# Kernel optimization log

Hardware: AMD Instinct MI355X
Metric: run time of the kernel (lower is better)

## Reference

```python
import jax, jax.numpy as jnp
import numpy as np
from jax import lax

B, T, P, H, O = 64, 96, 256, 128, 24  # batch, seq_len, num_points, hidden_dim, pred_len


def setup_inputs() -> dict:
    key = jax.random.key(0)
    ks = jax.random.split(key, 7)
    s = 1.0 / np.sqrt(H)  # torch LSTM/Linear default init scale
    return {
        "x": jax.random.normal(ks[0], (B, T, P, 1), dtype=jnp.float32),
        "W_ih": jax.random.uniform(ks[1], (P, 4 * H, 1), jnp.float32, -s, s),
        "W_hh": jax.random.uniform(ks[2], (P, 4 * H, H), jnp.float32, -s, s),
        "b_ih": jax.random.uniform(ks[3], (P, 4 * H), jnp.float32, -s, s),
        "b_hh": jax.random.uniform(ks[4], (P, 4 * H), jnp.float32, -s, s),
        "W_fc": jax.random.uniform(ks[5], (P, O, H), jnp.float32, -s, s),
        "b_fc": jax.random.uniform(ks[6], (P, O), jnp.float32, -s, s),
    }


def reference(x, W_ih, W_hh, b_ih, b_hh, W_fc, b_fc):
    # x: [B, T, P, F]; model uses only feature 0
    xs = x[..., 0]  # [B, T, P]
    # input_dim == 1, so input-to-gate contribution is a scaled broadcast of W_ih
    # precompute for all timesteps: [T, B, P, 4H]
    gx = jnp.einsum("btp,pg->tbpg", xs, W_ih[:, :, 0]) + (b_ih + b_hh)

    def step(carry, gxt):
        h, c = carry  # [B, P, H] each
        gates = gxt + jnp.einsum("bph,pgh->bpg", h, W_hh)  # [B, P, 4H]
        i, f, g, o = jnp.split(gates, 4, axis=-1)  # torch gate order i,f,g,o
        i = jax.nn.sigmoid(i)
        f = jax.nn.sigmoid(f)
        g = jnp.tanh(g)
        o = jax.nn.sigmoid(o)
        c = f * c + i * g
        h = o * jnp.tanh(c)
        return (h, c), None

    h0 = jnp.zeros((B, P, H), dtype=x.dtype)
    (h, _), _ = lax.scan(step, (h0, h0), gx)
    # per-point Linear on final hidden state: [B, P, O]
    out = jnp.einsum("bph,poh->bpo", h, W_fc) + b_fc
    # original stacks point outputs on last dim -> [B, pred_len, P]
    return jnp.transpose(out, (0, 2, 1))
```

## Files before the change

kernel.cpp:

```cpp
#include <hip/hip_runtime.h>
#include <hip/hip_bf16.h>

#define Bdim 64
#define Tdim 96
#define Pdim 256
#define Hdim 128
#define Gdim 512
#define Odim 24
#define BH   32
#define WROW 132

typedef _Float16 f16x8 __attribute__((ext_vector_type(8)));
typedef float    f32x16 __attribute__((ext_vector_type(16)));

union H8 { uint2 u2[2]; unsigned short s[8]; _Float16 h[8]; f16x8 v; };
union HS { _Float16 h; unsigned short s; };

__device__ __forceinline__ float exp2_fast(float x) {
#if __has_builtin(__builtin_amdgcn_exp2f)
    return __builtin_amdgcn_exp2f(x);
#else
    return __expf(x * 0.6931471805599453f);
#endif
}

__global__ __launch_bounds__(512, 4)
void lstm_fused(const float* __restrict__ x,
                const float* __restrict__ W_ih,
                const float* __restrict__ W_hh,
                const float* __restrict__ b_ih,
                const float* __restrict__ b_hh,
                const float* __restrict__ W_fc,
                const float* __restrict__ b_fc,
                float* __restrict__ out)
{
    __shared__ unsigned short hl[2][BH * WROW];

    const int p    = blockIdx.x >> 1;
    const int half = blockIdx.x & 1;
    const int tid  = threadIdx.x;
    const int w    = tid >> 6;
    const int l    = tid & 63;
    const int l31  = l & 31;
    const int hi   = l >> 5;

    const float L1 = 1.4426950408889634f;
    const float L2 = 2.0f * L1;

    for (int i = tid; i < 2 * BH * WROW; i += 512) ((unsigned short*)hl)[i] = 0;

    f16x8 afr[2][9];
    #pragma unroll
    for (int mt = 0; mt < 2; ++mt) {
        const int rp   = w * 64 + mt * 32 + l31;
        const int orow = ((rp & 3) << 7) | (rp >> 2);
        const float sc = ((rp & 3) == 2) ? L2 : L1;
        const float* rowp = W_hh + (size_t)p * Gdim * Hdim + (size_t)orow * Hdim;
        #pragma unroll
        for (int ks = 0; ks < 8; ++ks) {
            int k0 = ks * 16 + hi * 8;
            float4 va = *(const float4*)(rowp + k0);
            float4 vb = *(const float4*)(rowp + k0 + 4);
            H8 u;
            u.h[0] = (_Float16)(sc * va.x); u.h[1] = (_Float16)(sc * va.y);
            u.h[2] = (_Float16)(sc * va.z); u.h[3] = (_Float16)(sc * va.w);
            u.h[4] = (_Float16)(sc * vb.x); u.h[5] = (_Float16)(sc * vb.y);
            u.h[6] = (_Float16)(sc * vb.z); u.h[7] = (_Float16)(sc * vb.w);
            afr[mt][ks] = u.v;
        }
        H8 u9;
        #pragma unroll
        for (int j = 0; j < 8; ++j) u9.s[j] = 0;
        if (hi == 0) {
            u9.h[0] = (_Float16)(sc * W_ih[(size_t)p * Gdim + orow]);
            u9.h[1] = (_Float16)(sc * (b_ih[(size_t)p * Gdim + orow] +
                                       b_hh[(size_t)p * Gdim + orow]));
        }
        afr[mt][8] = u9.v;
    }

    float cre[2][4];
    #pragma unroll
    for (int mt = 0; mt < 2; ++mt)
        #pragma unroll
        for (int q = 0; q < 4; ++q) cre[mt][q] = 0.f;

    const float* xp = x + (size_t)((half * BH + l31) * Tdim) * Pdim + p;
    float xv = xp[0];

    __syncthreads();

    int cur = 0;
    for (int t = 0; t < Tdim; ++t) {
        float xn = (t + 1 < Tdim) ? xp[(size_t)(t + 1) * Pdim] : 0.f;

        f32x16 acc[2];
        #pragma unroll
        for (int j = 0; j < 16; ++j) { acc[0][j] = 0.f; acc[1][j] = 0.f; }

        const char* hbase = (const char*)hl[cur];
        #pragma unroll
        for (int ks = 0; ks < 8; ++ks) {
            int boff = l31 * (WROW * 2) + ks * 32 + hi * 16;
            H8 b0;
            b0.u2[0] = *(const uint2*)(hbase + boff);
            b0.u2[1] = *(const uint2*)(hbase + boff + 8);
            acc[0] = __builtin_amdgcn_mfma_f32_32x32x16_f16(afr[0][ks], b0.v, acc[0], 0, 0, 0);
            acc[1] = __builtin_amdgcn_mfma_f32_32x32x16_f16(afr[1][ks], b0.v, acc[1], 0, 0, 0);
        }
        {
            H8 b0;
            #pragma unroll
            for (int j = 0; j < 8; ++j) b0.s[j] = 0;
            if (hi == 0) { b0.h[0] = (_Float16)xv; b0.h[1] = (_Float16)1.0f; }
            acc[0] = __builtin_amdgcn_mfma_f32_32x32x16_f16(afr[0][8], b0.v, acc[0], 0, 0, 0);
            acc[1] = __builtin_amdgcn_mfma_f32_32x32x16_f16(afr[1][8], b0.v, acc[1], 0, 0, 0);
        }

        unsigned short* hw = hl[cur ^ 1];
        #pragma unroll
        for (int mt = 0; mt < 2; ++mt) {
            #pragma unroll
            for (int q = 0; q < 4; ++q) {
                float yi = acc[mt][4 * q + 0];
                float yf = acc[mt][4 * q + 1];
                float yg = acc[mt][4 * q + 2];
                float yo = acc[mt][4 * q + 3];
                float Ef = exp2_fast(-yf);
                float Ei = exp2_fast(-yi);
                float Eg = exp2_fast(yg);
                float t1 = 1.0f + Ef;
                float t2 = 1.0f + Ei;
                float t3 = Eg + 1.0f;
                float t4 = Eg - 1.0f;
                float den = (t1 * t2) * t3;
                float ct2 = cre[mt][q] * t2;
                float g4  = L2 * t4;
                float num = __builtin_fmaf(ct2, t3, g4 * t1);
                float cn  = num * __builtin_amdgcn_rcpf(den);
                cn = fminf(60.0f, fmaxf(-60.0f, cn));
                cre[mt][q] = cn;
                float Eo = exp2_fast(-yo);
                float Ec = exp2_fast(cn);
                float den2 = (1.0f + Eo) * (Ec + 1.0f);
                float hv = (Ec - 1.0f) * __builtin_amdgcn_rcpf(den2);
                HS hs; hs.h = (_Float16)hv;
                int k = w * 16 + mt * 8 + 2 * q + hi;
                hw[l31 * WROW + k] = hs.s;
            }
        }

        __syncthreads();
        cur ^= 1;
        xv = xn;
    }

    const float* wfc = W_fc + (size_t)p * Odim * Hdim;
    const float* bfc = b_fc + (size_t)p * Odim;
    const unsigned short* hf = hl[cur];
    for (int i = tid; i < BH * Odim; i += 512) {
        int o = i % Odim;
        int b = i / Odim;
        float s = bfc[o];
        const float* wr = wfc + o * Hdim;
        const unsigned short* hr = hf + b * WROW;
        #pragma unroll 8
        for (int k2 = 0; k2 < Hdim; ++k2) {
            HS hs; hs.s = hr[k2];
            s = __builtin_fmaf(wr[k2], (float)hs.h, s);
        }
        int bg = half * BH + b;
        out[(size_t)bg * Odim * Pdim + (size_t)o * Pdim + p] = s;
    }
}

extern "C" void kernel_launch(void* const* d_in, const int* in_sizes, int n_in,
                              void* d_out, int out_size, void* d_ws, size_t ws_size,
                              hipStream_t stream) {
    const float* x    = (const float*)d_in[0];
    const float* W_ih = (const float*)d_in[1];
    const float* W_hh = (const float*)d_in[2];
    const float* b_ih = (const float*)d_in[3];
    const float* b_hh = (const float*)d_in[4];
    const float* W_fc = (const float*)d_in[5];
    const float* b_fc = (const float*)d_in[6];
    float* out = (float*)d_out;

    lstm_fused<<<dim3(2 * Pdim), dim3(512), 0, stream>>>(x, W_ih, W_hh, b_ih, b_hh, W_fc, b_fc, out);
}
```

Before: 419.3 us.

## Merge batch halves into one block and interleave GEMM with the other half's epilogue

```diff
diff --git a/kernel.cpp b/kernel.cpp
--- a/kernel.cpp
+++ b/kernel.cpp
@@ -24,7 +24,7 @@
 #endif
 }
 
-__global__ __launch_bounds__(512, 4)
+__global__ __launch_bounds__(1024, 4)
 void lstm_fused(const float* __restrict__ x,
                 const float* __restrict__ W_ih,
                 const float* __restrict__ W_hh,
@@ -34,25 +34,22 @@
                 const float* __restrict__ b_fc,
                 float* __restrict__ out)
 {
-    __shared__ unsigned short hl[2][BH * WROW];
+    __shared__ unsigned short hs[2][2][BH * WROW];
 
-    const int p    = blockIdx.x >> 1;
-    const int half = blockIdx.x & 1;
-    const int tid  = threadIdx.x;
-    const int w    = tid >> 6;
-    const int l    = tid & 63;
-    const int l31  = l & 31;
-    const int hi   = l >> 5;
+    const int p   = blockIdx.x;
+    const int tid = threadIdx.x;
+    const int w   = tid >> 6;
+    const int l31 = tid & 31;
+    const int hi  = (tid >> 5) & 1;
 
     const float L1 = 1.4426950408889634f;
     const float L2 = 2.0f * L1;
 
-    for (int i = tid; i < 2 * BH * WROW; i += 512) ((unsigned short*)hl)[i] = 0;
+    for (int i = tid; i < 2 * 2 * BH * WROW; i += 1024) ((unsigned short*)hs)[i] = 0;
 
-    f16x8 afr[2][9];
-    #pragma unroll
-    for (int mt = 0; mt < 2; ++mt) {
-        const int rp   = w * 64 + mt * 32 + l31;
+    f16x8 afr[9];
+    {
+        const int rp   = w * 32 + l31;
         const int orow = ((rp & 3) << 7) | (rp >> 2);
         const float sc = ((rp & 3) == 2) ? L2 : L1;
         const float* rowp = W_hh + (size_t)p * Gdim * Hdim + (size_t)orow * Hdim;
@@ -66,7 +63,7 @@
             u.h[2] = (_Float16)(sc * va.z); u.h[3] = (_Float16)(sc * va.w);
             u.h[4] = (_Float16)(sc * vb.x); u.h[5] = (_Float16)(sc * vb.y);
             u.h[6] = (_Float16)(sc * vb.z); u.h[7] = (_Float16)(sc * vb.w);
-            afr[mt][ks] = u.v;
+            afr[ks] = u.v;
         }
         H8 u9;
         #pragma unroll
@@ -76,101 +73,101 @@
             u9.h[1] = (_Float16)(sc * (b_ih[(size_t)p * Gdim + orow] +
                                        b_hh[(size_t)p * Gdim + orow]));
         }
-        afr[mt][8] = u9.v;
+        afr[8] = u9.v;
     }
 
-    float cre[2][4];
-    #pragma unroll
-    for (int mt = 0; mt < 2; ++mt)
+    auto do_gemm = [&](const unsigned short* hb, float xv) -> f32x16 {
+        f32x16 a;
         #pragma unroll
-        for (int q = 0; q < 4; ++q) cre[mt][q] = 0.f;
+        for (int j = 0; j < 16; ++j) a[j] = 0.f;
+        const char* hbase = (const char*)hb;
+        #pragma unroll
+        for (int ks = 0; ks < 8; ++ks) {
+            int boff = l31 * (WROW * 2) + ks * 32 + hi * 16;
+            H8 bb;
+            bb.u2[0] = *(const uint2*)(hbase + boff);
+            bb.u2[1] = *(const uint2*)(hbase + boff + 8);
+            a = __builtin_amdgcn_mfma_f32_32x32x16_f16(afr[ks], bb.v, a, 0, 0, 0);
+        }
+        H8 bg;
+        #pragma unroll
+        for (int j = 0; j < 8; ++j) bg.s[j] = 0;
+        if (hi == 0) { bg.h[0] = (_Float16)xv; bg.h[1] = (_Float16)1.0f; }
+        a = __builtin_amdgcn_mfma_f32_32x32x16_f16(afr[8], bg.v, a, 0, 0, 0);
+        return a;
+    };
 
-    const float* xp = x + (size_t)((half * BH + l31) * Tdim) * Pdim + p;
-    float xv = xp[0];
+    auto do_ep = [&](const f32x16& a, float* cr, unsigned short* hw) {
+        #pragma unroll
+        for (int q = 0; q < 4; ++q) {
+            float yi = a[4 * q + 0];
+            float yf = a[4 * q + 1];
+            float yg = a[4 * q + 2];
+            float yo = a[4 * q + 3];
+            float Ef = exp2_fast(-yf);
+            float Ei = exp2_fast(-yi);
+            float Eg = exp2_fast(yg);
+            float t1 = 1.0f + Ef;
+            float t2 = 1.0f + Ei;
+            float t3 = Eg + 1.0f;
+            float t4 = Eg - 1.0f;
+            float den = (t1 * t2) * t3;
+            float num = __builtin_fmaf(cr[q] * t2, t3, (L2 * t4) * t1);
+            float cn  = num * __builtin_amdgcn_rcpf(den);
+            cn = fminf(60.0f, fmaxf(-60.0f, cn));
+            cr[q] = cn;
+            float Eo = exp2_fast(-yo);
+            float Ec = exp2_fast(cn);
+            float hv = (Ec - 1.0f) * __builtin_amdgcn_rcpf((1.0f + Eo) * (Ec + 1.0f));
+            HS s2; s2.h = (_Float16)hv;
+            hw[l31 * WROW + (w * 8 + 2 * q + hi)] = s2.s;
+        }
+    };
+
+    float cre0[4] = {0.f, 0.f, 0.f, 0.f};
+    float cre1[4] = {0.f, 0.f, 0.f, 0.f};
+
+    const float* xp0 = x + (size_t)((0 * BH + l31) * Tdim) * Pdim + p;
+    const float* xp1 = x + (size_t)((1 * BH + l31) * Tdim) * Pdim + p;
+    float xv0 = xp0[0];
+    float xv1 = xp1[0];
 
     __syncthreads();
 
-    int cur = 0;
+    int b0 = 0, b1 = 0;
+    f32x16 acc0 = do_gemm(hs[0][b0], xv0);
+    xv0 = xp0[(size_t)1 * Pdim];
+
+    f32x16 acc1;
     for (int t = 0; t < Tdim; ++t) {
-        float xn = (t + 1 < Tdim) ? xp[(size_t)(t + 1) * Pdim] : 0.f;
+        acc1 = do_gemm(hs[1][b1], xv1);
+        do_ep(acc0, cre0, hs[0][b0 ^ 1]);
+        __syncthreads();
+        b0 ^= 1;
+        xv1 = (t + 1 < Tdim) ? xp1[(size_t)(t + 1) * Pdim] : 0.f;
 
-        f32x16 acc[2];
-        #pragma unroll
-        for (int j = 0; j < 16; ++j) { acc[0][j] = 0.f; acc[1][j] = 0.f; }
-
-        const char* hbase = (const char*)hl[cur];
-        #pragma unroll
-        for (int ks = 0; ks < 8; ++ks) {
-            int boff = l31 * (WROW * 2) + ks * 32 + hi * 16;
-            H8 b0;
-            b0.u2[0] = *(const uint2*)(hbase + boff);
-            b0.u2[1] = *(const uint2*)(hbase + boff + 8);
-            acc[0] = __builtin_amdgcn_mfma_f32_32x32x16_f16(afr[0][ks], b0.v, acc[0], 0, 0, 0);
-            acc[1] = __builtin_amdgcn_mfma_f32_32x32x16_f16(afr[1][ks], b0.v, acc[1], 0, 0, 0);
-        }
-        {
-            H8 b0;
-            #pragma unroll
-            for (int j = 0; j < 8; ++j) b0.s[j] = 0;
-            if (hi == 0) { b0.h[0] = (_Float16)xv; b0.h[1] = (_Float16)1.0f; }
-            acc[0] = __builtin_amdgcn_mfma_f32_32x32x16_f16(afr[0][8], b0.v, acc[0], 0, 0, 0);
-            acc[1] = __builtin_amdgcn_mfma_f32_32x32x16_f16(afr[1][8], b0.v, acc[1], 0, 0, 0);
-        }
-
-        unsigned short* hw = hl[cur ^ 1];
-        #pragma unroll
-        for (int mt = 0; mt < 2; ++mt) {
-            #pragma unroll
-            for (int q = 0; q < 4; ++q) {
-                float yi = acc[mt][4 * q + 0];
-                float yf = acc[mt][4 * q + 1];
-                float yg = acc[mt][4 * q + 2];
-                float yo = acc[mt][4 * q + 3];
-                float Ef = exp2_fast(-yf);
-                float Ei = exp2_fast(-yi);
-                float Eg = exp2_fast(yg);
-                float t1 = 1.0f + Ef;
-                float t2 = 1.0f + Ei;
-                float t3 = Eg + 1.0f;
-                float t4 = Eg - 1.0f;
-                float den = (t1 * t2) * t3;
-                float ct2 = cre[mt][q] * t2;
-                float g4  = L2 * t4;
-                float num = __builtin_fmaf(ct2, t3, g4 * t1);
-                float cn  = num * __builtin_amdgcn_rcpf(den);
-                cn = fminf(60.0f, fmaxf(-60.0f, cn));
-                cre[mt][q] = cn;
-                float Eo = exp2_fast(-yo);
-                float Ec = exp2_fast(cn);
-                float den2 = (1.0f + Eo) * (Ec + 1.0f);
-                float hv = (Ec - 1.0f) * __builtin_amdgcn_rcpf(den2);
-                HS hs; hs.h = (_Float16)hv;
-                int k = w * 16 + mt * 8 + 2 * q + hi;
-                hw[l31 * WROW + k] = hs.s;
-            }
-        }
-
+        acc0 = do_gemm(hs[0][b0], xv0);
+        do_ep(acc1, cre1, hs[1][b1 ^ 1]);
         __syncthreads();
-        cur ^= 1;
-        xv = xn;
+        b1 ^= 1;
+        xv0 = (t + 2 < Tdim) ? xp0[(size_t)(t + 2) * Pdim] : 0.f;
     }
 
     const float* wfc = W_fc + (size_t)p * Odim * Hdim;
     const float* bfc = b_fc + (size_t)p * Odim;
-    const unsigned short* hf = hl[cur];
-    for (int i = tid; i < BH * Odim; i += 512) {
+    for (int i = tid; i < Bdim * Odim; i += 1024) {
         int o = i % Odim;
         int b = i / Odim;
+        const unsigned short* hr = (b < BH) ? (hs[0][b0] + b * WROW)
+                                            : (hs[1][b1] + (b - BH) * WROW);
         float s = bfc[o];
         const float* wr = wfc + o * Hdim;
-        const unsigned short* hr = hf + b * WROW;
         #pragma unroll 8
         for (int k2 = 0; k2 < Hdim; ++k2) {
-            HS hs; hs.s = hr[k2];
-            s = __builtin_fmaf(wr[k2], (float)hs.h, s);
+            HS s2; s2.s = hr[k2];
+            s = __builtin_fmaf(wr[k2], (float)s2.h, s);
         }
-        int bg = half * BH + b;
-        out[(size_t)bg * Odim * Pdim + (size_t)o * Pdim + p] = s;
+        out[(size_t)b * Odim * Pdim + (size_t)o * Pdim + p] = s;
     }
 }
 
@@ -186,5 +183,5 @@
     const float* b_fc = (const float*)d_in[6];
     float* out = (float*)d_out;
 
-    lstm_fused<<<dim3(2 * Pdim), dim3(512), 0, stream>>>(x, W_ih, W_hh, b_ih, b_hh, W_fc, b_fc, out);
+    lstm_fused<<<dim3(Pdim), dim3(1024), 0, stream>>>(x, W_ih, W_hh, b_ih, b_hh, W_fc, b_fc, out);
 }
```

After: 400.4 us. -4.5%, faster.
